# Optimization experiments

Measured on AMD Instinct MI355X. Metric: run time of the kernel, lower is better.

Reference implementation:

```python
import jax, jax.numpy as jnp
import numpy as np

IN_C = 64
K = 3          # kernel_size
PAD = K // 2   # padding for offset_conv and deformconv


def conv2d(x, w, b, pad):
    # x: [B,C,H,W], w: [O,I,kh,kw] (OIHW), stride 1
    y = jax.lax.conv_general_dilated(
        x, w, (1, 1), [(pad, pad), (pad, pad)],
        dimension_numbers=('NCHW', 'OIHW', 'NCHW'))
    return y + b[None, :, None, None]


def deform_conv2d(x, offset, w, b, pad):
    # torchvision DeformConv2d (v1, no modulation), stride=1, dilation=1.
    # x: [B,Cin,H,W]; offset: [B,2*K*K,H,W] as (dy,dx) pairs per kernel tap
    # (row-major tap order); w: [Cout,Cin,K,K]; b: [Cout].
    B, Cin, H, W = x.shape
    Kh = w.shape[-1]
    K2 = Kh * Kh
    off = offset.reshape(B, K2, 2, H, W)
    dy, dx = off[:, :, 0], off[:, :, 1]                     # [B,K2,H,W]

    ky = (jnp.arange(K2) // Kh).astype(x.dtype)             # kernel tap rows
    kx = (jnp.arange(K2) % Kh).astype(x.dtype)              # kernel tap cols
    base_y = jnp.arange(H, dtype=x.dtype)[None, :, None] - pad + ky[:, None, None]  # [K2,H,1]
    base_x = jnp.arange(W, dtype=x.dtype)[None, None, :] - pad + kx[:, None, None]  # [K2,1,W]
    py = base_y[None] + dy                                  # [B,K2,H,W] sample y
    px = base_x[None] + dx                                  # [B,K2,H,W] sample x

    y0 = jnp.floor(py)
    x0 = jnp.floor(px)
    wy1 = py - y0; wy0 = 1.0 - wy1                          # bilinear weights
    wx1 = px - x0; wx0 = 1.0 - wx1

    x_flat = x.reshape(B, Cin, H * W)

    def gather(iy, ix):
        # zero-padded bilinear corner gather -> [B,Cin,K2,H,W]
        valid = (iy >= 0) & (iy < H) & (ix >= 0) & (ix < W)
        iyc = jnp.clip(iy, 0, H - 1).astype(jnp.int32)
        ixc = jnp.clip(ix, 0, W - 1).astype(jnp.int32)
        flat = (iyc * W + ixc).reshape(B, -1)               # [B,K2*H*W]
        g = jax.vmap(lambda xb, ib: xb[:, ib])(x_flat, flat)
        g = g.reshape(B, Cin, K2, H, W)
        return g * valid.reshape(B, 1, K2, H, W).astype(x.dtype)

    val = (gather(y0,       x0      ) * (wy0 * wx0)[:, None]
         + gather(y0,       x0 + 1.0) * (wy0 * wx1)[:, None]
         + gather(y0 + 1.0, x0      ) * (wy1 * wx0)[:, None]
         + gather(y0 + 1.0, x0 + 1.0) * (wy1 * wx1)[:, None])  # [B,Cin,K2,H,W]

    out = jnp.einsum('bckhw,ock->bohw', val, w.reshape(w.shape[0], Cin, K2))
    return out + b[None, :, None, None]


def setup_inputs() -> dict:
    key = jax.random.key(0)
    ks = jax.random.split(key, 7)
    B, H, W = 2, 256, 256
    f32 = jnp.float32
    x = jax.random.normal(ks[0], (B, IN_C, H, W), f32)
    # ConvTranspose2d weight layout: [in_c, out_c=64, K, K]
    w_deconv = jax.random.normal(ks[1], (IN_C, 64, K, K), f32) * 0.05
    b_deconv = jax.random.normal(ks[2], (64,), f32) * 0.05
    w_off = jax.random.normal(ks[3], (2 * K * K, 64, K, K), f32) * 0.05
    b_off = jax.random.normal(ks[4], (2 * K * K,), f32) * 0.05
    w_def = jax.random.normal(ks[5], (IN_C, 64, K, K), f32) * 0.05
    b_def = jax.random.normal(ks[6], (IN_C,), f32) * 0.05
    return {'x': x, 'w_deconv': w_deconv, 'b_deconv': b_deconv,
            'w_off': w_off, 'b_off': b_off, 'w_def': w_def, 'b_def': b_def}


def reference(x, w_deconv, b_deconv, w_off, b_off, w_def, b_def):
    # ConvTranspose2d(stride=1, pad=1) == conv with flipped, IO-transposed
    # weights and padding K-1-1 = 1.
    wt = jnp.flip(w_deconv, (2, 3)).transpose(1, 0, 2, 3)   # [64, in_c, K, K]
    h = jax.nn.relu(conv2d(x, wt, b_deconv, K - 1 - 1))
    offset = conv2d(h, w_off, b_off, PAD)
    out = deform_conv2d(h, offset, w_def, b_def, PAD)
    return jax.nn.relu(out)
```

## Files before the change

### kernel.cpp

```cpp
#include <hip/hip_runtime.h>

#define H_ 256
#define W_ 256
#define HW_ (H_*W_)

typedef __attribute__((ext_vector_type(8))) short bf16x8;
typedef __attribute__((ext_vector_type(4))) float f32x4;

__device__ __forceinline__ float bflo(unsigned u) { return __builtin_bit_cast(float, u << 16); }
__device__ __forceinline__ float bfhi(unsigned u) { return __builtin_bit_cast(float, u & 0xffff0000u); }
__device__ __forceinline__ unsigned f2bf(float f) {
    unsigned b = __builtin_bit_cast(unsigned, f);
    b += 0x7fffu + ((b >> 16) & 1u);
    return b >> 16;
}
__device__ __forceinline__ unsigned cvtpk(float lo, float hi) {
    unsigned r;
    asm("v_cvt_pk_bf16_f32 %0, %1, %2" : "=v"(r) : "v"(lo), "v"(hi));
    return r;
}
__device__ __forceinline__ void unpack8(uint4 v, float* f) {
    f[0] = bflo(v.x); f[1] = bfhi(v.x); f[2] = bflo(v.y); f[3] = bfhi(v.y);
    f[4] = bflo(v.z); f[5] = bfhi(v.z); f[6] = bflo(v.w); f[7] = bfhi(v.w);
}

__global__ void prep_weights(const float* __restrict__ wdef, unsigned short* __restrict__ wdefb,
                             const float* __restrict__ wdc, unsigned short* __restrict__ wdcb,
                             const float* __restrict__ woff, unsigned short* __restrict__ woffb) {
    int idx = blockIdx.x * 256 + threadIdx.x;
    if (idx < 36864) {
        int k = idx >> 12, o = (idx >> 6) & 63, c = idx & 63;
        wdefb[idx] = (unsigned short)f2bf(wdef[(o * 64 + c) * 9 + k]);
        wdcb[idx]  = (unsigned short)f2bf(wdc[(c * 64 + o) * 9 + (8 - k)]);
    }
    if (idx < 18432) {
        int k = idx >> 11, o = (idx >> 6) & 31, c = idx & 63;
        woffb[idx] = (o < 18) ? (unsigned short)f2bf(woff[(o * 64 + c) * 9 + k])
                              : (unsigned short)0;
    }
}

__global__ __launch_bounds__(256) void x_to_nhwc(const float* __restrict__ x,
                                                 unsigned short* __restrict__ xb) {
    __shared__ unsigned short t[64 * 72];
    int tid = threadIdx.x;
    int b = blockIdx.x >> 10;
    long pxb = (long)(blockIdx.x & 1023) * 64;
    const float* xp = x + (long)b * 64 * HW_ + pxb;
    int px = tid & 63, cg = tid >> 6;
    for (int c = cg; c < 64; c += 4)
        t[px * 72 + c] = (unsigned short)f2bf(xp[(long)c * HW_ + px]);
    __syncthreads();
    int spx = tid >> 2, q = tid & 3;
    unsigned short* dst = xb + ((long)b * HW_ + pxb + spx) * 64 + q * 16;
    *(uint4*)dst       = *(const uint4*)&t[spx * 72 + q * 16];
    *(uint4*)(dst + 8) = *(const uint4*)&t[spx * 72 + q * 16 + 8];
}

__device__ __forceinline__ void stage_row(const unsigned short* __restrict__ src,
                                          unsigned short* lds, int X0, int tid) {
    for (int e = tid; e < 1040; e += 256) {
        int i = e >> 3, q = e & 7;
        int col = X0 - 1 + i;
        uint4 v = { 0u, 0u, 0u, 0u };
        if (col >= 0 && col < W_) v = *(const uint4*)&src[(long)col * 64 + q * 8];
        *(uint4*)&lds[i * 72 + q * 8] = v;
    }
}

__global__ __launch_bounds__(256, 4) void conv1_mfma(const unsigned short* __restrict__ xb,
                                                     const unsigned short* __restrict__ wdcb,
                                                     const float* __restrict__ bias,
                                                     unsigned short* __restrict__ h) {
    __shared__ __align__(16) unsigned short sA[130 * 72];

    int tid = threadIdx.x;
    int linear = (blockIdx.x & 7) * 128 + (blockIdx.x >> 3);
    int bx = linear & 1;
    int y  = (linear >> 1) & 255;
    int b  = linear >> 9;
    int X0 = bx * 128;

    int wave = tid >> 6, lane = tid & 63;
    int lr = lane & 15, lg = lane >> 4;
    int n0 = wave * 16;

    f32x4 acc[8];
#pragma unroll
    for (int m = 0; m < 8; ++m) { acc[m][0]=0.f; acc[m][1]=0.f; acc[m][2]=0.f; acc[m][3]=0.f; }

    const unsigned short* xbb = xb + (long)b * HW_ * 64;
    const unsigned short* pb  = wdcb + (n0 + lr) * 64 + lg * 8;

    for (int ky = 0; ky < 3; ++ky) {
        int yr = y + ky - 1;
        if (yr < 0 || yr >= H_) continue;
        __syncthreads();
        stage_row(xbb + (long)yr * (W_ * 64), sA, X0, tid);
        __syncthreads();
#pragma unroll
        for (int kx = 0; kx < 3; ++kx) {
            int k = ky * 3 + kx;
            bf16x8 b0 = *(const bf16x8*)(pb + k * 4096);
            bf16x8 b1 = *(const bf16x8*)(pb + k * 4096 + 32);
#pragma unroll
            for (int m = 0; m < 8; ++m) {
                const unsigned short* ap = &sA[(m * 16 + lr + kx) * 72 + lg * 8];
                bf16x8 a0 = *(const bf16x8*)ap;
                bf16x8 a1 = *(const bf16x8*)(ap + 32);
                acc[m] = __builtin_amdgcn_mfma_f32_16x16x32_bf16(a0, b0, acc[m], 0, 0, 0);
                acc[m] = __builtin_amdgcn_mfma_f32_16x16x32_bf16(a1, b1, acc[m], 0, 0, 0);
            }
        }
    }

    __syncthreads();
    float bv = bias[n0 + lr];
#pragma unroll
    for (int m = 0; m < 8; ++m)
#pragma unroll
        for (int r = 0; r < 4; ++r) {
            float vv = fmaxf(acc[m][r] + bv, 0.f);
            sA[(m * 16 + lg * 4 + r) * 72 + n0 + lr] = (unsigned short)f2bf(vv);
        }
    __syncthreads();
    int spx = tid >> 1, sc0 = (tid & 1) * 32;
    unsigned short* dst = h + ((long)b * HW_ + (long)y * W_ + X0 + spx) * 64 + sc0;
    const unsigned short* srcp = &sA[spx * 72 + sc0];
#pragma unroll
    for (int q = 0; q < 4; ++q)
        *(uint4*)(dst + q * 8) = *(const uint4*)(srcp + q * 8);
}

__global__ __launch_bounds__(256, 4) void conv2_mfma(const unsigned short* __restrict__ h,
                                                     const unsigned short* __restrict__ woffb,
                                                     const float* __restrict__ bias,
                                                     float* __restrict__ off) {
    __shared__ __align__(16) unsigned short sA[130 * 72];

    int tid = threadIdx.x;
    int linear = (blockIdx.x & 7) * 128 + (blockIdx.x >> 3);
    int bx = linear & 1;
    int y  = (linear >> 1) & 255;
    int b  = linear >> 9;
    int X0 = bx * 128;

    int wave = tid >> 6, lane = tid & 63;
    int lr = lane & 15, lg = lane >> 4;
    int pxh = wave & 1, nh = wave >> 1;
    int n0 = nh * 16;
    int pxb = pxh * 64;

    f32x4 acc[4];
#pragma unroll
    for (int m = 0; m < 4; ++m) { acc[m][0]=0.f; acc[m][1]=0.f; acc[m][2]=0.f; acc[m][3]=0.f; }

    const unsigned short* hb = h + (long)b * HW_ * 64;
    const unsigned short* pb = woffb + (n0 + lr) * 64 + lg * 8;

    for (int ky = 0; ky < 3; ++ky) {
        int yr = y + ky - 1;
        if (yr < 0 || yr >= H_) continue;
        __syncthreads();
        stage_row(hb + (long)yr * (W_ * 64), sA, X0, tid);
        __syncthreads();
#pragma unroll
        for (int kx = 0; kx < 3; ++kx) {
            int k = ky * 3 + kx;
            bf16x8 b0 = *(const bf16x8*)(pb + k * 2048);
            bf16x8 b1 = *(const bf16x8*)(pb + k * 2048 + 32);
#pragma unroll
            for (int m = 0; m < 4; ++m) {
                const unsigned short* ap = &sA[(pxb + m * 16 + lr + kx) * 72 + lg * 8];
                bf16x8 a0 = *(const bf16x8*)ap;
                bf16x8 a1 = *(const bf16x8*)(ap + 32);
                acc[m] = __builtin_amdgcn_mfma_f32_16x16x32_bf16(a0, b0, acc[m], 0, 0, 0);
                acc[m] = __builtin_amdgcn_mfma_f32_16x16x32_bf16(a1, b1, acc[m], 0, 0, 0);
            }
        }
    }

    int o = n0 + lr;
    if (o < 18) {
        float bv = bias[o];
        float* op = off + ((long)b * 18 + o) * HW_ + (long)y * W_ + X0 + pxb;
#pragma unroll
        for (int m = 0; m < 4; ++m) {
            float4 r = { acc[m][0] + bv, acc[m][1] + bv, acc[m][2] + bv, acc[m][3] + bv };
            *(float4*)(op + m * 16 + lg * 4) = r;
        }
    }
}

struct Pass16 {
    uint4 a00, a01, a10, a11;
    uint4 b00, b01, b10, b11;
    float w00, w01, w10, w11;
};

__device__ __forceinline__ Pass16 issue16(const unsigned short* __restrict__ hb,
                                          int k, int y, int px, float dy, float dx, int c0) {
    Pass16 s;
    float py  = (float)(y - 1 + k / 3) + dy;
    float pxs = (float)(px - 1 + k % 3) + dx;
    float y0f = floorf(py), x0f = floorf(pxs);
    int iy0 = (int)y0f, ix0 = (int)x0f;
    float wy1 = py - y0f, wx1 = pxs - x0f;
    float wy0 = 1.f - wy1, wx0 = 1.f - wx1;
    bool vy0 = (iy0 >= 0) && (iy0 < H_);
    bool vy1 = (iy0 >= -1) && (iy0 < H_ - 1);
    bool vx0 = (ix0 >= 0) && (ix0 < W_);
    bool vx1 = (ix0 >= -1) && (ix0 < W_ - 1);
    int cy0 = min(max(iy0, 0), H_ - 1), cy1 = min(max(iy0 + 1, 0), H_ - 1);
    int cx0 = min(max(ix0, 0), W_ - 1), cx1 = min(max(ix0 + 1, 0), W_ - 1);
    s.w00 = wy0 * wx0 * ((vy0 && vx0) ? 1.f : 0.f);
    s.w01 = wy0 * wx1 * ((vy0 && vx1) ? 1.f : 0.f);
    s.w10 = wy1 * wx0 * ((vy1 && vx0) ? 1.f : 0.f);
    s.w11 = wy1 * wx1 * ((vy1 && vx1) ? 1.f : 0.f);
    int r00 = (cy0 * W_ + cx0) * 64 + c0, r01 = (cy0 * W_ + cx1) * 64 + c0;
    int r10 = (cy1 * W_ + cx0) * 64 + c0, r11 = (cy1 * W_ + cx1) * 64 + c0;
    s.a00 = *(const uint4*)&hb[r00];     s.a01 = *(const uint4*)&hb[r01];
    s.a10 = *(const uint4*)&hb[r10];     s.a11 = *(const uint4*)&hb[r11];
    s.b00 = *(const uint4*)&hb[r00 + 8]; s.b01 = *(const uint4*)&hb[r01 + 8];
    s.b10 = *(const uint4*)&hb[r10 + 8]; s.b11 = *(const uint4*)&hb[r11 + 8];
    return s;
}

__device__ __forceinline__ uint4 interp8u(uint4 q0, uint4 q1, uint4 q2, uint4 q3,
                                          float w00, float w01, float w10, float w11) {
    float g0[8], g1[8], g2[8], g3[8];
    unpack8(q0, g0); unpack8(q1, g1); unpack8(q2, g2); unpack8(q3, g3);
    unsigned r[4];
#pragma unroll
    for (int j = 0; j < 4; ++j) {
        float lo = fmaf(g3[2*j],   w11, fmaf(g2[2*j],   w10, fmaf(g1[2*j],   w01, g0[2*j]   * w00)));
        float hi = fmaf(g3[2*j+1], w11, fmaf(g2[2*j+1], w10, fmaf(g1[2*j+1], w01, g0[2*j+1] * w00)));
        r[j] = cvtpk(lo, hi);
    }
    uint4 u = { r[0], r[1], r[2], r[3] };
    return u;
}

__global__ __launch_bounds__(256, 4) void deform_mfma(const unsigned short* __restrict__ h,
                                                      const float* __restrict__ off,
                                                      const unsigned short* __restrict__ wdefb,
                                                      const float* __restrict__ bias,
                                                      float* __restrict__ out) {
    __shared__ __align__(16) unsigned short val[2][64 * 64];

    int tid = threadIdx.x;
    int linear = (blockIdx.x & 7) * 256 + (blockIdx.x >> 3);
    int b  = linear >> 10;
    int y  = (linear >> 2) & 255;
    int x0 = (linear & 3) * 64;

    int lane = tid & 63, wave = tid >> 6;
    int lr = lane & 15, lg = lane >> 4;
    int n0 = wave * 16;
    int gpx = tid >> 2;
    int gc  = tid & 3;
    int c0  = gc * 16;
    int gx  = x0 + gpx;

    f32x4 acc[4];
#pragma unroll
    for (int m = 0; m < 4; ++m) { acc[m][0]=0.f; acc[m][1]=0.f; acc[m][2]=0.f; acc[m][3]=0.f; }

    const unsigned short* hb   = h + (long)b * HW_ * 64;
    const float* ofb  = off + (long)b * 18 * HW_ + y * W_ + gx;
    const unsigned short* bsrc = wdefb + (n0 + lr) * 64 + lg * 8;

    float dy0 = ofb[0], dx0 = ofb[HW_];
    Pass16 S = issue16(hb, 0, y, gx, dy0, dx0, c0);
    float dyn = ofb[2 * HW_], dxn = ofb[3 * HW_];
    bf16x8 bc0 = *(const bf16x8*)bsrc;
    bf16x8 bc1 = *(const bf16x8*)(bsrc + 32);

    int slotL = ((2 * gc)     ^ (gpx & 7)) * 8;
    int slotH = ((2 * gc + 1) ^ (gpx & 7)) * 8;
    int rdL   = ((lg)     ^ (lr & 7)) * 8;
    int rdH   = ((lg + 4) ^ (lr & 7)) * 8;

    for (int k = 0; k < 9; ++k) {
        Pass16 S2;
        bf16x8 bn0 = bc0, bn1 = bc1;
        float dy3 = 0.f, dx3 = 0.f;
        if (k < 8) {
            S2  = issue16(hb, k + 1, y, gx, dyn, dxn, c0);
            bn0 = *(const bf16x8*)(bsrc + (k + 1) * 4096);
            bn1 = *(const bf16x8*)(bsrc + (k + 1) * 4096 + 32);
            if (k < 7) { dy3 = ofb[(2 * k + 4) * HW_]; dx3 = ofb[(2 * k + 5) * HW_]; }
        }

        unsigned short* vb = val[k & 1];
        *(uint4*)&vb[gpx * 64 + slotL] = interp8u(S.a00, S.a01, S.a10, S.a11,
                                                  S.w00, S.w01, S.w10, S.w11);
        *(uint4*)&vb[gpx * 64 + slotH] = interp8u(S.b00, S.b01, S.b10, S.b11,
                                                  S.w00, S.w01, S.w10, S.w11);

        asm volatile("s_waitcnt lgkmcnt(0)" ::: "memory");
        __builtin_amdgcn_s_barrier();
        asm volatile("" ::: "memory");

        __builtin_amdgcn_s_setprio(1);
#pragma unroll
        for (int m = 0; m < 4; ++m) {
            const unsigned short* ap = &vb[(m * 16 + lr) * 64];
            bf16x8 a0 = *(const bf16x8*)&ap[rdL];
            bf16x8 a1 = *(const bf16x8*)&ap[rdH];
            acc[m] = __builtin_amdgcn_mfma_f32_16x16x32_bf16(a0, bc0, acc[m], 0, 0, 0);
            acc[m] = __builtin_amdgcn_mfma_f32_16x16x32_bf16(a1, bc1, acc[m], 0, 0, 0);
        }
        __builtin_amdgcn_s_setprio(0);

        S = S2; bc0 = bn0; bc1 = bn1; dyn = dy3; dxn = dx3;
    }

    float bv = bias[n0 + lr];
    float* outb = out + ((long)b * 64 + n0 + lr) * HW_ + y * W_ + x0;
#pragma unroll
    for (int m = 0; m < 4; ++m) {
        float4 r = { fmaxf(acc[m][0] + bv, 0.f), fmaxf(acc[m][1] + bv, 0.f),
                     fmaxf(acc[m][2] + bv, 0.f), fmaxf(acc[m][3] + bv, 0.f) };
        *(float4*)(outb + m * 16 + lg * 4) = r;
    }
}

extern "C" void kernel_launch(void* const* d_in, const int* in_sizes, int n_in,
                              void* d_out, int out_size, void* d_ws, size_t ws_size,
                              hipStream_t stream) {
    const float* x        = (const float*)d_in[0];
    const float* w_deconv = (const float*)d_in[1];
    const float* b_deconv = (const float*)d_in[2];
    const float* w_off    = (const float*)d_in[3];
    const float* b_off    = (const float*)d_in[4];
    const float* w_def    = (const float*)d_in[5];
    const float* b_def    = (const float*)d_in[6];
    float* out = (float*)d_out;

    char* ws = (char*)d_ws;
    unsigned short* xbb   = (unsigned short*)ws;
    unsigned short* hbf   = (unsigned short*)(ws + 16777216);
    float* offset         = (float*)(ws + 33554432);
    unsigned short* wdcb  = (unsigned short*)(ws + 42991616);
    unsigned short* wdefb = (unsigned short*)(ws + 43065344);
    unsigned short* woffb = (unsigned short*)(ws + 43139072);

    prep_weights<<<144, 256, 0, stream>>>(w_def, wdefb, w_deconv, wdcb, w_off, woffb);
    x_to_nhwc<<<2048, 256, 0, stream>>>(x, xbb);
    conv1_mfma<<<1024, 256, 0, stream>>>(xbb, wdcb, b_deconv, hbf);
    conv2_mfma<<<1024, 256, 0, stream>>>(hbf, woffb, b_off, offset);
    deform_mfma<<<2048, 256, 0, stream>>>(hbf, offset, wdefb, b_def, out);
}
```

Measured before the change: 110.5 us.

## Double-buffer LDS row staging with register prefetch in conv kernels

Both 3x3 conv kernels now load the next input row into registers while the current row is in LDS. They use two LDS buffers, so each row step needs only one barrier instead of two. The aim is to hide global-load latency behind the MFMA work. The deform kernel's tap loop is also fully unrolled. In exchange, LDS use doubles (about 37 KB per block), which may limit occupancy, and register pressure rises from the prefetch buffer and the unrolling.

```diff
diff --git a/kernel.cpp b/kernel.cpp
--- a/kernel.cpp
+++ b/kernel.cpp
@@ -57,22 +57,11 @@
     *(uint4*)(dst + 8) = *(const uint4*)&t[spx * 72 + q * 16 + 8];
 }
 
-__device__ __forceinline__ void stage_row(const unsigned short* __restrict__ src,
-                                          unsigned short* lds, int X0, int tid) {
-    for (int e = tid; e < 1040; e += 256) {
-        int i = e >> 3, q = e & 7;
-        int col = X0 - 1 + i;
-        uint4 v = { 0u, 0u, 0u, 0u };
-        if (col >= 0 && col < W_) v = *(const uint4*)&src[(long)col * 64 + q * 8];
-        *(uint4*)&lds[i * 72 + q * 8] = v;
-    }
-}
-
 __global__ __launch_bounds__(256, 4) void conv1_mfma(const unsigned short* __restrict__ xb,
                                                      const unsigned short* __restrict__ wdcb,
                                                      const float* __restrict__ bias,
                                                      unsigned short* __restrict__ h) {
-    __shared__ __align__(16) unsigned short sA[130 * 72];
+    __shared__ __align__(16) unsigned short sA[2][130 * 72];
 
     int tid = threadIdx.x;
     int linear = (blockIdx.x & 7) * 128 + (blockIdx.x >> 3);
@@ -92,12 +81,38 @@
     const unsigned short* xbb = xb + (long)b * HW_ * 64;
     const unsigned short* pb  = wdcb + (n0 + lr) * 64 + lg * 8;
 
-    for (int ky = 0; ky < 3; ++ky) {
-        int yr = y + ky - 1;
-        if (yr < 0 || yr >= H_) continue;
-        __syncthreads();
-        stage_row(xbb + (long)yr * (W_ * 64), sA, X0, tid);
-        __syncthreads();
+    int r0 = (y == 0) ? 1 : 0;
+    int r1 = (y == H_ - 1) ? 1 : 2;
+
+    uint4 L[5];
+    auto LOADROW = [&](int yr) {
+        const unsigned short* src = xbb + (long)yr * (W_ * 64);
+#pragma unroll
+        for (int t = 0; t < 5; ++t) {
+            int e = tid + t * 256;
+            uint4 v = { 0u, 0u, 0u, 0u };
+            if (e < 1040) {
+                int col = X0 - 1 + (e >> 3);
+                if (col >= 0 && col < W_)
+                    v = *(const uint4*)&src[(long)col * 64 + (e & 7) * 8];
+            }
+            L[t] = v;
+        }
+    };
+
+    LOADROW(y + r0 - 1);
+    int pa = 0;
+    for (int ky = r0; ky <= r1; ++ky, ++pa) {
+        unsigned short* buf = sA[pa & 1];
+#pragma unroll
+        for (int t = 0; t < 5; ++t) {
+            int e = tid + t * 256;
+            if (e < 1040) *(uint4*)&buf[(e >> 3) * 72 + (e & 7) * 8] = L[t];
+        }
+        if (ky < r1) LOADROW(y + ky);
+        asm volatile("s_waitcnt lgkmcnt(0)" ::: "memory");
+        __builtin_amdgcn_s_barrier();
+        asm volatile("" ::: "memory");
 #pragma unroll
         for (int kx = 0; kx < 3; ++kx) {
             int k = ky * 3 + kx;
@@ -105,7 +120,7 @@
             bf16x8 b1 = *(const bf16x8*)(pb + k * 4096 + 32);
 #pragma unroll
             for (int m = 0; m < 8; ++m) {
-                const unsigned short* ap = &sA[(m * 16 + lr + kx) * 72 + lg * 8];
+                const unsigned short* ap = &buf[(m * 16 + lr + kx) * 72 + lg * 8];
                 bf16x8 a0 = *(const bf16x8*)ap;
                 bf16x8 a1 = *(const bf16x8*)(ap + 32);
                 acc[m] = __builtin_amdgcn_mfma_f32_16x16x32_bf16(a0, b0, acc[m], 0, 0, 0);
@@ -116,17 +131,18 @@
 
     __syncthreads();
     float bv = bias[n0 + lr];
+    unsigned short* cs = sA[0];
 #pragma unroll
     for (int m = 0; m < 8; ++m)
 #pragma unroll
         for (int r = 0; r < 4; ++r) {
             float vv = fmaxf(acc[m][r] + bv, 0.f);
-            sA[(m * 16 + lg * 4 + r) * 72 + n0 + lr] = (unsigned short)f2bf(vv);
+            cs[(m * 16 + lg * 4 + r) * 72 + n0 + lr] = (unsigned short)f2bf(vv);
         }
     __syncthreads();
     int spx = tid >> 1, sc0 = (tid & 1) * 32;
     unsigned short* dst = h + ((long)b * HW_ + (long)y * W_ + X0 + spx) * 64 + sc0;
-    const unsigned short* srcp = &sA[spx * 72 + sc0];
+    const unsigned short* srcp = &cs[spx * 72 + sc0];
 #pragma unroll
     for (int q = 0; q < 4; ++q)
         *(uint4*)(dst + q * 8) = *(const uint4*)(srcp + q * 8);
@@ -136,7 +152,7 @@
                                                      const unsigned short* __restrict__ woffb,
                                                      const float* __restrict__ bias,
                                                      float* __restrict__ off) {
-    __shared__ __align__(16) unsigned short sA[130 * 72];
+    __shared__ __align__(16) unsigned short sA[2][130 * 72];
 
     int tid = threadIdx.x;
     int linear = (blockIdx.x & 7) * 128 + (blockIdx.x >> 3);
@@ -158,12 +174,38 @@
     const unsigned short* hb = h + (long)b * HW_ * 64;
     const unsigned short* pb = woffb + (n0 + lr) * 64 + lg * 8;
 
-    for (int ky = 0; ky < 3; ++ky) {
-        int yr = y + ky - 1;
-        if (yr < 0 || yr >= H_) continue;
-        __syncthreads();
-        stage_row(hb + (long)yr * (W_ * 64), sA, X0, tid);
-        __syncthreads();
+    int r0 = (y == 0) ? 1 : 0;
+    int r1 = (y == H_ - 1) ? 1 : 2;
+
+    uint4 L[5];
+    auto LOADROW = [&](int yr) {
+        const unsigned short* src = hb + (long)yr * (W_ * 64);
+#pragma unroll
+        for (int t = 0; t < 5; ++t) {
+            int e = tid + t * 256;
+            uint4 v = { 0u, 0u, 0u, 0u };
+            if (e < 1040) {
+                int col = X0 - 1 + (e >> 3);
+                if (col >= 0 && col < W_)
+                    v = *(const uint4*)&src[(long)col * 64 + (e & 7) * 8];
+            }
+            L[t] = v;
+        }
+    };
+
+    LOADROW(y + r0 - 1);
+    int pa = 0;
+    for (int ky = r0; ky <= r1; ++ky, ++pa) {
+        unsigned short* buf = sA[pa & 1];
+#pragma unroll
+        for (int t = 0; t < 5; ++t) {
+            int e = tid + t * 256;
+            if (e < 1040) *(uint4*)&buf[(e >> 3) * 72 + (e & 7) * 8] = L[t];
+        }
+        if (ky < r1) LOADROW(y + ky);
+        asm volatile("s_waitcnt lgkmcnt(0)" ::: "memory");
+        __builtin_amdgcn_s_barrier();
+        asm volatile("" ::: "memory");
 #pragma unroll
         for (int kx = 0; kx < 3; ++kx) {
             int k = ky * 3 + kx;
@@ -171,7 +213,7 @@
             bf16x8 b1 = *(const bf16x8*)(pb + k * 2048 + 32);
 #pragma unroll
             for (int m = 0; m < 4; ++m) {
-                const unsigned short* ap = &sA[(pxb + m * 16 + lr + kx) * 72 + lg * 8];
+                const unsigned short* ap = &buf[(pxb + m * 16 + lr + kx) * 72 + lg * 8];
                 bf16x8 a0 = *(const bf16x8*)ap;
                 bf16x8 a1 = *(const bf16x8*)(ap + 32);
                 acc[m] = __builtin_amdgcn_mfma_f32_16x16x32_bf16(a0, b0, acc[m], 0, 0, 0);
@@ -281,6 +323,7 @@
     int rdL   = ((lg)     ^ (lr & 7)) * 8;
     int rdH   = ((lg + 4) ^ (lr & 7)) * 8;
 
+#pragma unroll
     for (int k = 0; k < 9; ++k) {
         Pass16 S2;
         bf16x8 bn0 = bc0, bn1 = bc1;
```

New measurement: 113.5 us. 2.7% more time.
